# Performance work log

Hardware: AMD Instinct MI355X
Metric: run time of the kernel (lower is better)

The kernel has to match this reference:

```python
import jax, jax.numpy as jnp
import numpy as np

EPS = 1e-12  # F.normalize default eps


def _sage_conv(x, src, dst, num_nodes, W_l, W_r, b):
    # mean-aggregate neighbor features: for each dst node, mean over x[src]
    agg = jax.ops.segment_sum(x[src], dst, num_segments=num_nodes)  # [N, d_in]
    cnt = jax.ops.segment_sum(jnp.ones((src.shape[0],), x.dtype), dst,
                              num_segments=num_nodes)
    mean = agg / jnp.maximum(cnt, 1.0)[:, None]
    # PyG SAGEConv: lin_l(aggregated) + bias + lin_r(root)
    return mean @ W_l + b + x @ W_r


def setup_inputs() -> dict:
    key = jax.random.key(0)
    ks = jax.random.split(key, 10)
    N, E, F_in = 50000, 400000, 128
    x = jax.random.normal(ks[0], (N, F_in), dtype=jnp.float32)
    edge_index = jax.random.randint(ks[1], (2, E), 0, N, dtype=jnp.int64)

    def lin(k, din, dout):
        s = 1.0 / np.sqrt(din)
        return jax.random.uniform(k, (din, dout), jnp.float32, -s, s)

    params = {
        "W1_l": lin(ks[2], F_in, 2048), "W1_r": lin(ks[3], F_in, 2048),
        "b1": jnp.zeros((2048,), jnp.float32),
        "W2_l": lin(ks[4], 2048, 2048), "W2_r": lin(ks[5], 2048, 2048),
        "b2": jnp.zeros((2048,), jnp.float32),
        "W3_l": lin(ks[6], 2048, 1024), "W3_r": lin(ks[7], 2048, 1024),
        "b3": jnp.zeros((1024,), jnp.float32),
    }
    return {"x": x, "unused": 0, "edge_index": edge_index, **params}


def reference(x, unused, edge_index,
              W1_l, W1_r, b1, W2_l, W2_r, b2, W3_l, W3_r, b3):
    del unused
    N = x.shape[0]
    src, dst = edge_index[0], edge_index[1]
    h = jax.nn.relu(_sage_conv(x, src, dst, N, W1_l, W1_r, b1))
    h = jax.nn.relu(_sage_conv(h, src, dst, N, W2_l, W2_r, b2))
    h = jax.nn.relu(_sage_conv(h, src, dst, N, W3_l, W3_r, b3))
    # F.normalize(dim=1): x / max(||x||_2, eps)
    norm = jnp.linalg.norm(h, axis=1, keepdims=True)
    return h / jnp.maximum(norm, EPS)
```

## Files before the change

kernel.cpp:

```cpp
#include <hip/hip_runtime.h>
#include <stdint.h>

#define NN 50000
#define EE 400000

typedef unsigned short u16;
typedef __attribute__((ext_vector_type(8))) short bf16x8;
typedef __attribute__((ext_vector_type(4))) float f32x4;
typedef __attribute__((address_space(3))) uint32_t lds_u32_t;
typedef __attribute__((address_space(1))) uint32_t glob_u32_t;

__device__ inline float bf2f(u16 u) {
  union { uint32_t i; float f; } x; x.i = ((uint32_t)u) << 16; return x.f;
}
__device__ inline u16 f2bf(float f) {
  union { float f; uint32_t i; } x; x.f = f;
  x.i += 0x7fffu + ((x.i >> 16) & 1u);
  return (u16)(x.i >> 16);
}
__device__ inline void gload_lds16(const void* g, void* l) {
  __builtin_amdgcn_global_load_lds((const glob_u32_t*)g, (lds_u32_t*)l, 16, 0, 0);
}

__global__ void detect_i64(const int* __restrict__ e, int* __restrict__ flag) {
  __shared__ int sh[256];
  int t = threadIdx.x;
  int v = 0;
  for (int i = t; i < 4096; i += 256) v |= e[2 * i + 1];
  sh[t] = v; __syncthreads();
  for (int s = 128; s > 0; s >>= 1) { if (t < s) sh[t] |= sh[t + s]; __syncthreads(); }
  if (t == 0) flag[0] = (sh[0] == 0) ? 1 : 0;
}

__global__ void conv_edges(const int* __restrict__ e, const int* __restrict__ flag,
                           int* __restrict__ src, int* __restrict__ dst) {
  int i = blockIdx.x * 256 + threadIdx.x;
  if (i >= EE) return;
  if (flag[0]) { src[i] = e[2 * i]; dst[i] = e[2 * (EE + i)]; }
  else         { src[i] = e[i];     dst[i] = e[EE + i]; }
}

__global__ void count_edges(const int* __restrict__ dst, int* __restrict__ cnt) {
  int i = blockIdx.x * 256 + threadIdx.x;
  if (i < EE) atomicAdd(&cnt[dst[i]], 1);
}

__global__ void scan_counts(const int* __restrict__ cnt, int* __restrict__ offs,
                            int* __restrict__ cursor) {
  __shared__ int sh[1024];
  __shared__ int carry_sh;
  int tid = threadIdx.x;
  if (tid == 0) carry_sh = 0;
  __syncthreads();
  int nChunks = (NN + 1023) / 1024;
  for (int c = 0; c < nChunks; ++c) {
    int idx = c * 1024 + tid;
    int v = (idx < NN) ? cnt[idx] : 0;
    sh[tid] = v; __syncthreads();
    for (int off = 1; off < 1024; off <<= 1) {
      int t = (tid >= off) ? sh[tid - off] : 0;
      __syncthreads();
      sh[tid] += t;
      __syncthreads();
    }
    int incl = sh[tid];
    int excl = incl - v + carry_sh;
    if (idx < NN) { offs[idx] = excl; cursor[idx] = excl; }
    __syncthreads();
    if (tid == 0) carry_sh += sh[1023];
    __syncthreads();
  }
}

__global__ void fill_buckets(const int* __restrict__ src, const int* __restrict__ dst,
                             int* __restrict__ cursor, int* __restrict__ bucket) {
  int i = blockIdx.x * 256 + threadIdx.x;
  if (i >= EE) return;
  int p = atomicAdd(&cursor[dst[i]], 1);
  bucket[p] = src[i];
}

__global__ void cvt_bf16(const float* __restrict__ in, u16* __restrict__ out, int n4) {
  int i = blockIdx.x * 256 + threadIdx.x;
  if (i >= n4) return;
  float4 v = ((const float4*)in)[i];
  u16 o[4] = { f2bf(v.x), f2bf(v.y), f2bf(v.z), f2bf(v.w) };
  uint2 pack;
  pack.x = (uint32_t)o[0] | ((uint32_t)o[1] << 16);
  pack.y = (uint32_t)o[2] | ((uint32_t)o[3] << 16);
  ((uint2*)out)[i] = pack;
}

__global__ void transposeW(const float* __restrict__ W, u16* __restrict__ Wt,
                           int K, int Nc) {
  __shared__ float tile[32][33];
  int n0 = blockIdx.x * 32, k0 = blockIdx.y * 32;
  int tx = threadIdx.x, ty = threadIdx.y;
  #pragma unroll
  for (int i = 0; i < 4; ++i)
    tile[ty + i * 8][tx] = W[(size_t)(k0 + ty + i * 8) * Nc + n0 + tx];
  __syncthreads();
  #pragma unroll
  for (int i = 0; i < 4; ++i)
    Wt[(size_t)(n0 + ty + i * 8) * K + k0 + tx] = f2bf(tile[tx][ty + i * 8]);
}

template<int D>
__global__ void agg_mean(const u16* __restrict__ h, const int* __restrict__ offs,
                         const int* __restrict__ cnt, const int* __restrict__ bucket,
                         u16* __restrict__ outp) {
  int node = blockIdx.x;
  int t = threadIdx.x;
  int base = t * 8;
  if (base >= D) return;
  int start = offs[node];
  int c = cnt[node];
  float acc[8];
  #pragma unroll
  for (int i = 0; i < 8; ++i) acc[i] = 0.f;
  for (int j = 0; j < c; ++j) {
    int s = bucket[start + j];
    uint4 q = *(const uint4*)(h + (size_t)s * D + base);
    acc[0] += bf2f((u16)(q.x & 0xffff)); acc[1] += bf2f((u16)(q.x >> 16));
    acc[2] += bf2f((u16)(q.y & 0xffff)); acc[3] += bf2f((u16)(q.y >> 16));
    acc[4] += bf2f((u16)(q.z & 0xffff)); acc[5] += bf2f((u16)(q.z >> 16));
    acc[6] += bf2f((u16)(q.w & 0xffff)); acc[7] += bf2f((u16)(q.w >> 16));
  }
  float inv = 1.0f / fmaxf((float)c, 1.0f);
  uint4 o;
  o.x = (uint32_t)f2bf(acc[0] * inv) | ((uint32_t)f2bf(acc[1] * inv) << 16);
  o.y = (uint32_t)f2bf(acc[2] * inv) | ((uint32_t)f2bf(acc[3] * inv) << 16);
  o.z = (uint32_t)f2bf(acc[4] * inv) | ((uint32_t)f2bf(acc[5] * inv) << 16);
  o.w = (uint32_t)f2bf(acc[6] * inv) | ((uint32_t)f2bf(acc[7] * inv) << 16);
  *(uint4*)(outp + (size_t)node * D + base) = o;
}


template<int K>
__device__ inline void stage_half(char* ldsX, const u16* __restrict__ G, int grow0,
                                  int k0, int h, int wave, int lrow8, int slot8,
                                  int clampR) {
  #pragma unroll
  for (int j = 0; j < 2; ++j) {
    const int lrow = h * 128 + j * 64 + wave * 8;
    int gr = grow0 + lrow + lrow8;
    gr = gr < clampR ? gr : clampR - 1;
    gload_lds16(G + (size_t)gr * K + k0 + slot8, ldsX + lrow * 128);
  }
}

#define LOAD_A(BASE, MH)                                                        \
  _Pragma("unroll") for (int mf = 0; mf < 4; ++mf) {                            \
    af[mf][0] = *(const bf16x8*)((BASE) + ((MH) * 128 + mf * 16) * 128 + kc0);  \
    af[mf][1] = *(const bf16x8*)((BASE) + ((MH) * 128 + mf * 16) * 128 + kc1);  \
  }
#define LOAD_B(DST, BASE, NH)                                                   \
  _Pragma("unroll") for (int nf = 0; nf < 2; ++nf) {                            \
    DST[nf][0] = *(const bf16x8*)((BASE) + ((NH) * 128 + nf * 16) * 128 + kc0); \
    DST[nf][1] = *(const bf16x8*)((BASE) + ((NH) * 128 + nf * 16) * 128 + kc1); \
  }
#define QUAD(MH, BREG, NH)                                                      \
  _Pragma("unroll") for (int mf = 0; mf < 4; ++mf)                              \
  _Pragma("unroll") for (int nf = 0; nf < 2; ++nf) {                            \
    acc[(MH)*4+mf][(NH)*2+nf] = __builtin_amdgcn_mfma_f32_16x16x32_bf16(        \
        af[mf][0], BREG[nf][0], acc[(MH)*4+mf][(NH)*2+nf], 0, 0, 0);            \
    acc[(MH)*4+mf][(NH)*2+nf] = __builtin_amdgcn_mfma_f32_16x16x32_bf16(        \
        af[mf][1], BREG[nf][1], acc[(MH)*4+mf][(NH)*2+nf], 0, 0, 0);            \
  }
#define BAR() __builtin_amdgcn_s_barrier()
#define LGKM0()                                                                 \
  do {                                                                          \
    asm volatile("s_waitcnt lgkmcnt(0)" ::: "memory");                          \
    __builtin_amdgcn_sched_barrier(0);                                          \
  } while (0)

template<int K, bool OUT_F32>
__global__ __launch_bounds__(512, 2)
void gemm8ph(const u16* __restrict__ A1, const u16* __restrict__ A2,
             const u16* __restrict__ B1t, const u16* __restrict__ B2t,
             const float* __restrict__ bias, void* __restrict__ Cout,
             int M, int Nc, int tilesN) {
  __shared__ __align__(16) char lds[131072];
  constexpr int NTp = K / 64;
  constexpr int NT = 2 * NTp;

  const int nwg = gridDim.x;
  const int bid = blockIdx.x;
  const int wg = (bid & 7) * (nwg >> 3) + (bid >> 3);
  const int bx = wg % tilesN, by = wg / tilesN;
  const int rowBase = by * 256, colBase = bx * 256;

  const int tid = threadIdx.x;
  const int lane = tid & 63;
  const int wave = tid >> 6;
  const int wm = wave >> 2, wn = wave & 3;
  const int r = lane & 15, kg = lane >> 4;
  const int sw = (r & 7) << 4;
  const int kc0 = (kg * 16) ^ sw;
  const int kc1 = (64 + kg * 16) ^ sw;
  const int slot8 = ((lane & 7) ^ ((lane >> 3) & 7)) * 8;
  const int lrow8 = lane >> 3;

  char* const pA0 = lds + (wm * 64 + r) * 128;
  char* const pB0 = lds + 32768 + (wn * 32 + r) * 128;

  f32x4 acc[8][4];
  #pragma unroll
  for (int m = 0; m < 8; ++m)
    #pragma unroll
    for (int n = 0; n < 4; ++n) acc[m][n] = (f32x4){0.f, 0.f, 0.f, 0.f};

  bf16x8 af[4][2], b0[2][2], b1[2][2];

  stage_half<K>(lds,         A1,  rowBase, 0, 0, wave, lrow8, slot8, M);
  stage_half<K>(lds + 32768, B1t, colBase, 0, 0, wave, lrow8, slot8, Nc);
  stage_half<K>(lds + 32768, B1t, colBase, 0, 1, wave, lrow8, slot8, Nc);
  stage_half<K>(lds,         A1,  rowBase, 0, 1, wave, lrow8, slot8, M);
  asm volatile("s_waitcnt vmcnt(2)" ::: "memory");
  BAR();

  for (int t = 0; t < NT - 1; ++t) {
    const int cur = t & 1;
    const char* cA = pA0 + cur * 65536;
    const char* cB = pB0 + cur * 65536;
    char* nA = lds + (cur ^ 1) * 65536;
    char* nB = nA + 32768;
    const int vt = t + 1;
    const u16* sA; const u16* sB; int sk0;
    if (vt >= NTp) { sA = A2; sB = B2t; sk0 = (vt - NTp) * 64; }
    else           { sA = A1; sB = B1t; sk0 = vt * 64; }

    LOAD_A(cA, 0); LOAD_B(b0, cB, 0); LOAD_B(b1, cB, 1);
    stage_half<K>(nA, sA, rowBase, sk0, 0, wave, lrow8, slot8, M);
    stage_half<K>(nB, sB, colBase, sk0, 0, wave, lrow8, slot8, Nc);
    BAR();
    LGKM0();
    __builtin_amdgcn_s_setprio(1);
    QUAD(0, b0, 0);
    QUAD(0, b1, 1);
    __builtin_amdgcn_s_setprio(0);
    asm volatile("s_waitcnt vmcnt(4)" ::: "memory");
    BAR();

    LOAD_A(cA, 1);
    stage_half<K>(nB, sB, colBase, sk0, 1, wave, lrow8, slot8, Nc);
    stage_half<K>(nA, sA, rowBase, sk0, 1, wave, lrow8, slot8, M);
    BAR();
    LGKM0();
    __builtin_amdgcn_s_setprio(1);
    QUAD(1, b1, 1);
    QUAD(1, b0, 0);
    __builtin_amdgcn_s_setprio(0);
    asm volatile("s_waitcnt vmcnt(2)" ::: "memory");
    BAR();
  }

  {
    const int cur = (NT - 1) & 1;
    const char* cA = pA0 + cur * 65536;
    const char* cB = pB0 + cur * 65536;

    LOAD_A(cA, 0); LOAD_B(b0, cB, 0); LOAD_B(b1, cB, 1);
    BAR();
    LGKM0();
    __builtin_amdgcn_s_setprio(1);
    QUAD(0, b0, 0);
    QUAD(0, b1, 1);
    __builtin_amdgcn_s_setprio(0);
    asm volatile("s_waitcnt vmcnt(0)" ::: "memory");
    BAR();

    LOAD_A(cA, 1);
    LGKM0();
    __builtin_amdgcn_s_setprio(1);
    QUAD(1, b1, 1);
    QUAD(1, b0, 0);
    __builtin_amdgcn_s_setprio(0);
  }

  const int q = lane >> 4;
  #pragma unroll
  for (int m = 0; m < 8; ++m) {
    int row = rowBase + (m >> 2) * 128 + wm * 64 + (m & 3) * 16 + q * 4;
    #pragma unroll
    for (int n = 0; n < 4; ++n) {
      int col = colBase + (n >> 1) * 128 + wn * 32 + (n & 1) * 16 + r;
      float bv = bias[col];
      #pragma unroll
      for (int reg = 0; reg < 4; ++reg) {
        if (row + reg < M) {
          float v = acc[m][n][reg] + bv;
          v = fmaxf(v, 0.f);
          if constexpr (OUT_F32)
            ((float*)Cout)[(size_t)(row + reg) * Nc + col] = v;
          else
            ((u16*)Cout)[(size_t)(row + reg) * Nc + col] = f2bf(v);
        }
      }
    }
  }
}

__global__ void l2norm_rows(float* __restrict__ out) {
  int node = blockIdx.x;
  int t = threadIdx.x;
  float4* p = (float4*)(out + (size_t)node * 1024);
  float4 v = p[t];
  float ss = v.x * v.x + v.y * v.y + v.z * v.z + v.w * v.w;
  #pragma unroll
  for (int off = 32; off > 0; off >>= 1) ss += __shfl_down(ss, off);
  __shared__ float sw[4];
  int lane = t & 63, w = t >> 6;
  if (lane == 0) sw[w] = ss;
  __syncthreads();
  float total = sw[0] + sw[1] + sw[2] + sw[3];
  float scale = 1.0f / fmaxf(sqrtf(total), 1e-12f);
  v.x *= scale; v.y *= scale; v.z *= scale; v.w *= scale;
  p[t] = v;
}

extern "C" void kernel_launch(void* const* d_in, const int* in_sizes, int n_in,
                              void* d_out, int out_size, void* d_ws, size_t ws_size,
                              hipStream_t stream) {
  const float* x   = (const float*)d_in[0];
  const int*   eix = (const int*)d_in[2];
  const float* W1l = (const float*)d_in[3];
  const float* W1r = (const float*)d_in[4];
  const float* b1  = (const float*)d_in[5];
  const float* W2l = (const float*)d_in[6];
  const float* W2r = (const float*)d_in[7];
  const float* b2  = (const float*)d_in[8];
  const float* W3l = (const float*)d_in[9];
  const float* W3r = (const float*)d_in[10];
  const float* b3  = (const float*)d_in[11];

  char* ws = (char*)d_ws;
  size_t off = 0;
  auto alloc = [&](size_t bytes) -> char* {
    char* p = ws + off;
    off += (bytes + 255) & ~(size_t)255;
    return p;
  };
  int* flag   = (int*)alloc(4);
  int* srcA   = (int*)alloc((size_t)EE * 4);
  int* dstA   = (int*)alloc((size_t)EE * 4);
  int* bucket = (int*)alloc((size_t)EE * 4);
  int* cnt    = (int*)alloc((size_t)NN * 4);
  int* offs   = (int*)alloc((size_t)NN * 4);
  int* cursor = (int*)alloc((size_t)NN * 4);
  u16* xb     = (u16*)alloc((size_t)NN * 128 * 2);
  u16* mean1  = (u16*)alloc((size_t)NN * 128 * 2);
  u16* W1lT   = (u16*)alloc((size_t)2048 * 128 * 2);
  u16* W1rT   = (u16*)alloc((size_t)2048 * 128 * 2);
  u16* W2lT   = (u16*)alloc((size_t)2048 * 2048 * 2);
  u16* W2rT   = (u16*)alloc((size_t)2048 * 2048 * 2);
  u16* W3lT   = (u16*)alloc((size_t)1024 * 2048 * 2);
  u16* W3rT   = (u16*)alloc((size_t)1024 * 2048 * 2);
  u16* bufA   = (u16*)alloc((size_t)NN * 2048 * 2);
  u16* bufB   = (u16*)alloc((size_t)NN * 2048 * 2);
  u16* mean2  = (u16*)d_out;

  detect_i64<<<1, 256, 0, stream>>>(eix, flag);
  conv_edges<<<(EE + 255) / 256, 256, 0, stream>>>(eix, flag, srcA, dstA);

  hipMemsetAsync(cnt, 0, (size_t)NN * 4, stream);
  count_edges<<<(EE + 255) / 256, 256, 0, stream>>>(dstA, cnt);
  scan_counts<<<1, 1024, 0, stream>>>(cnt, offs, cursor);
  fill_buckets<<<(EE + 255) / 256, 256, 0, stream>>>(srcA, dstA, cursor, bucket);

  cvt_bf16<<<(NN * 128 / 4 + 255) / 256, 256, 0, stream>>>(x, xb, NN * 128 / 4);
  transposeW<<<dim3(2048 / 32, 128 / 32), dim3(32, 8), 0, stream>>>(W1l, W1lT, 128, 2048);
  transposeW<<<dim3(2048 / 32, 128 / 32), dim3(32, 8), 0, stream>>>(W1r, W1rT, 128, 2048);
  transposeW<<<dim3(2048 / 32, 2048 / 32), dim3(32, 8), 0, stream>>>(W2l, W2lT, 2048, 2048);
  transposeW<<<dim3(2048 / 32, 2048 / 32), dim3(32, 8), 0, stream>>>(W2r, W2rT, 2048, 2048);
  transposeW<<<dim3(1024 / 32, 2048 / 32), dim3(32, 8), 0, stream>>>(W3l, W3lT, 2048, 1024);
  transposeW<<<dim3(1024 / 32, 2048 / 32), dim3(32, 8), 0, stream>>>(W3r, W3rT, 2048, 1024);

  const int tilesM = (NN + 255) / 256;

  agg_mean<128><<<NN, 64, 0, stream>>>(xb, offs, cnt, bucket, mean1);
  gemm8ph<128, false><<<tilesM * 8, 512, 0, stream>>>(
      mean1, xb, W1lT, W1rT, b1, bufA, NN, 2048, 8);

  agg_mean<2048><<<NN, 256, 0, stream>>>(bufA, offs, cnt, bucket, mean2);
  gemm8ph<2048, false><<<tilesM * 8, 512, 0, stream>>>(
      mean2, bufA, W2lT, W2rT, b2, bufB, NN, 2048, 8);

  agg_mean<2048><<<NN, 256, 0, stream>>>(bufB, offs, cnt, bucket, bufA);
  gemm8ph<2048, true><<<tilesM * 4, 512, 0, stream>>>(
      bufA, bufB, W3lT, W3rT, b3, d_out, NN, 1024, 4);

  l2norm_rows<<<NN, 256, 0, stream>>>((float*)d_out);
}
```

Before: 2.282 ms.

## Restructure GEMM main loop into four-phase pipeline with two-tile prefetch depth

Rewrites the bf16 GEMM main loop so each iteration splits into four compute phases, each interleaved with one half-tile global-to-LDS stage. Prefetch now runs two K-tiles ahead instead of one, with the LDS buffer being consumed refilled in pieces as it frees up. The sched_barrier in the LDS wait macro is removed. The goal is to hide global load latency better and spread memory traffic evenly across MFMA phases, at the cost of more barriers per iteration and tricky buffer-reuse hazards.

```diff
diff --git a/kernel.cpp b/kernel.cpp
--- a/kernel.cpp
+++ b/kernel.cpp
@@ -168,11 +168,7 @@
         af[mf][1], BREG[nf][1], acc[(MH)*4+mf][(NH)*2+nf], 0, 0, 0);            \
   }
 #define BAR() __builtin_amdgcn_s_barrier()
-#define LGKM0()                                                                 \
-  do {                                                                          \
-    asm volatile("s_waitcnt lgkmcnt(0)" ::: "memory");                          \
-    __builtin_amdgcn_sched_barrier(0);                                          \
-  } while (0)
+#define LGKM0() asm volatile("s_waitcnt lgkmcnt(0)" ::: "memory")
 
 template<int K, bool OUT_F32>
 __global__ __launch_bounds__(512, 2)
@@ -204,6 +200,12 @@
   char* const pA0 = lds + (wm * 64 + r) * 128;
   char* const pB0 = lds + 32768 + (wn * 32 + r) * 128;
 
+  auto tileSrc = [&](int v, const u16*& sA, const u16*& sB, int& k0) {
+    v = v < NT ? v : NT - 1;
+    if (v >= NTp) { sA = A2; sB = B2t; k0 = (v - NTp) * 64; }
+    else          { sA = A1; sB = B1t; k0 = v * 64; }
+  };
+
   f32x4 acc[8][4];
   #pragma unroll
   for (int m = 0; m < 8; ++m)
@@ -212,70 +214,71 @@
 
   bf16x8 af[4][2], b0[2][2], b1[2][2];
 
-  stage_half<K>(lds,         A1,  rowBase, 0, 0, wave, lrow8, slot8, M);
-  stage_half<K>(lds + 32768, B1t, colBase, 0, 0, wave, lrow8, slot8, Nc);
-  stage_half<K>(lds + 32768, B1t, colBase, 0, 1, wave, lrow8, slot8, Nc);
-  stage_half<K>(lds,         A1,  rowBase, 0, 1, wave, lrow8, slot8, M);
-  asm volatile("s_waitcnt vmcnt(2)" ::: "memory");
-  BAR();
-
-  for (int t = 0; t < NT - 1; ++t) {
-    const int cur = t & 1;
+  {
+    const u16 *sA0, *sB0, *sA1s, *sB1s; int k00, k01;
+    tileSrc(0, sA0, sB0, k00);
+    tileSrc(1, sA1s, sB1s, k01);
+    stage_half<K>(lds,                 sA0,  rowBase, k00, 0, wave, lrow8, slot8, M);
+    stage_half<K>(lds + 32768,         sB0,  colBase, k00, 0, wave, lrow8, slot8, Nc);
+    stage_half<K>(lds + 32768,         sB0,  colBase, k00, 1, wave, lrow8, slot8, Nc);
+    stage_half<K>(lds,                 sA0,  rowBase, k00, 1, wave, lrow8, slot8, M);
+    stage_half<K>(lds + 65536,         sA1s, rowBase, k01, 0, wave, lrow8, slot8, M);
+    stage_half<K>(lds + 65536 + 32768, sB1s, colBase, k01, 0, wave, lrow8, slot8, Nc);
+    stage_half<K>(lds + 65536 + 32768, sB1s, colBase, k01, 1, wave, lrow8, slot8, Nc);
+    asm volatile("s_waitcnt vmcnt(6)" ::: "memory");
+    BAR();
+  }
+
+  for (int u = 0; u < NT; ++u) {
+    const int cur = u & 1;
     const char* cA = pA0 + cur * 65536;
     const char* cB = pB0 + cur * 65536;
-    char* nA = lds + (cur ^ 1) * 65536;
-    char* nB = nA + 32768;
-    const int vt = t + 1;
-    const u16* sA; const u16* sB; int sk0;
-    if (vt >= NTp) { sA = A2; sB = B2t; sk0 = (vt - NTp) * 64; }
-    else           { sA = A1; sB = B1t; sk0 = vt * 64; }
-
-    LOAD_A(cA, 0); LOAD_B(b0, cB, 0); LOAD_B(b1, cB, 1);
-    stage_half<K>(nA, sA, rowBase, sk0, 0, wave, lrow8, slot8, M);
-    stage_half<K>(nB, sB, colBase, sk0, 0, wave, lrow8, slot8, Nc);
+    char* bufN = lds + (cur ^ 1) * 65536;
+    char* bufC = lds + cur * 65536;
+    const u16 *sAp1, *sBp1, *sAp2, *sBp2; int k0p1, k0p2;
+    tileSrc(u + 1, sAp1, sBp1, k0p1);
+    tileSrc(u + 2, sAp2, sBp2, k0p2);
+    const bool st1 = (u + 1 < NT), st2 = (u + 2 < NT);
+
+    LOAD_A(cA, 0); LOAD_B(b0, cB, 0);
+    if (st1) stage_half<K>(bufN, sAp1, rowBase, k0p1, 1, wave, lrow8, slot8, M);
+    asm volatile("s_waitcnt lgkmcnt(8)" ::: "memory");
     BAR();
     LGKM0();
     __builtin_amdgcn_s_setprio(1);
     QUAD(0, b0, 0);
+    __builtin_amdgcn_s_setprio(0);
+    BAR();
+
+    LOAD_B(b1, cB, 1);
+    if (st2) stage_half<K>(bufC, sAp2, rowBase, k0p2, 0, wave, lrow8, slot8, M);
+    BAR();
+    LGKM0();
+    __builtin_amdgcn_s_setprio(1);
     QUAD(0, b1, 1);
     __builtin_amdgcn_s_setprio(0);
-    asm volatile("s_waitcnt vmcnt(4)" ::: "memory");
     BAR();
 
     LOAD_A(cA, 1);
-    stage_half<K>(nB, sB, colBase, sk0, 1, wave, lrow8, slot8, Nc);
-    stage_half<K>(nA, sA, rowBase, sk0, 1, wave, lrow8, slot8, M);
+    if (st2) stage_half<K>(bufC + 32768, sBp2, colBase, k0p2, 0, wave, lrow8, slot8, Nc);
     BAR();
     LGKM0();
     __builtin_amdgcn_s_setprio(1);
     QUAD(1, b1, 1);
+    __builtin_amdgcn_s_setprio(0);
+    BAR();
+
+    if (st2) stage_half<K>(bufC + 32768, sBp2, colBase, k0p2, 1, wave, lrow8, slot8, Nc);
+    BAR();
+    __builtin_amdgcn_s_setprio(1);
     QUAD(1, b0, 0);
     __builtin_amdgcn_s_setprio(0);
-    asm volatile("s_waitcnt vmcnt(2)" ::: "memory");
-    BAR();
-  }
-
-  {
-    const int cur = (NT - 1) & 1;
-    const char* cA = pA0 + cur * 65536;
-    const char* cB = pB0 + cur * 65536;
-
-    LOAD_A(cA, 0); LOAD_B(b0, cB, 0); LOAD_B(b1, cB, 1);
-    BAR();
-    LGKM0();
-    __builtin_amdgcn_s_setprio(1);
-    QUAD(0, b0, 0);
-    QUAD(0, b1, 1);
-    __builtin_amdgcn_s_setprio(0);
-    asm volatile("s_waitcnt vmcnt(0)" ::: "memory");
-    BAR();
-
-    LOAD_A(cA, 1);
-    LGKM0();
-    __builtin_amdgcn_s_setprio(1);
-    QUAD(1, b1, 1);
-    QUAD(1, b0, 0);
-    __builtin_amdgcn_s_setprio(0);
+    if (u == NT - 2) {
+      asm volatile("s_waitcnt vmcnt(0)" ::: "memory");
+    } else if (u < NT - 2) {
+      asm volatile("s_waitcnt vmcnt(6)" ::: "memory");
+    }
+    BAR();
   }
 
   const int q = lane >> 4;
```

Result: faster. 2.210 ms (-3.2%).
